# Optimization experiments

Measured on AMD Instinct MI355X. Metric: run time of the kernel, lower is better.

The kernel has to match this reference:

```python
import jax, jax.numpy as jnp
import numpy as np

B, T, H = 2, 2048, 1024
NUM_HEADS = 16
HEAD_DIM = H // NUM_HEADS
MAX_REL = 4


def setup_inputs() -> dict:
    key = jax.random.key(0)
    ks = jax.random.split(key, 12)
    s = 1.0 / np.sqrt(H)
    inp = {
        "x": jax.random.normal(ks[0], (B, T, H), dtype=jnp.float32),
        "text_mask": jax.random.randint(ks[1], (B, T), 0, 2, dtype=jnp.int32),
        "Wq": jax.random.normal(ks[2], (H, H), dtype=jnp.float32) * s,
        "bq": jnp.zeros((H,), dtype=jnp.float32),
        "Wk": jax.random.normal(ks[3], (H, H), dtype=jnp.float32) * s,
        "bk": jnp.zeros((H,), dtype=jnp.float32),
        "Wv": jax.random.normal(ks[4], (H, H), dtype=jnp.float32) * s,
        "bv": jnp.zeros((H,), dtype=jnp.float32),
        "Wo": jax.random.normal(ks[5], (H, H), dtype=jnp.float32) * s,
        "bo": jnp.zeros((H,), dtype=jnp.float32),
        "rel_bias": jax.random.normal(ks[6], (2 * MAX_REL + 1, NUM_HEADS), dtype=jnp.float32),
    }
    return inp


def reference(x, text_mask, Wq, bq, Wk, bk, Wv, bv, Wo, bo, rel_bias):
    b, t, h = x.shape
    scale = HEAD_DIM ** (-0.5)

    def proj(W, bias):
        # [b,t,h] -> [b,heads,t,head_dim]
        return (x @ W.T + bias).reshape(b, t, NUM_HEADS, HEAD_DIM).transpose(0, 2, 1, 3)

    q = proj(Wq, bq)
    k = proj(Wk, bk)
    v = proj(Wv, bv)

    scores = jnp.einsum("bhqd,bhkd->bhqk", q, k) * scale  # [b,heads,t,t]

    pos = jnp.arange(t)
    rel = jnp.clip(pos[None, :] - pos[:, None], -MAX_REL, MAX_REL) + MAX_REL  # [t,t]
    bias = rel_bias[rel]  # [t,t,heads]
    scores = scores + bias.transpose(2, 0, 1)[None]  # broadcast over batch

    key_valid = text_mask.astype(bool)  # [b,t]
    scores = jnp.where(key_valid[:, None, None, :], scores, -10000.0)

    attn = jax.nn.softmax(scores, axis=-1)
    hidden = jnp.einsum("bhqk,bhkd->bhqd", attn, v)
    hidden = hidden.transpose(0, 2, 1, 3).reshape(b, t, h)
    out = hidden @ Wo.T + bo
    return out * text_mask.astype(out.dtype)[:, :, None]
```

## Files before the change

### kernel.cpp

```cpp
#include <hip/hip_runtime.h>
#include <hip/hip_bf16.h>

#define B_ 2
#define T_ 2048
#define H_ 1024
#define NH 16
#define HD 64

typedef __attribute__((ext_vector_type(8))) short bf16x8;
typedef __attribute__((ext_vector_type(4))) short bf16x4;
typedef __attribute__((ext_vector_type(4))) float f32x4;

#define ASYNC_COPY16(gptr, lptr)                                              \
    __builtin_amdgcn_global_load_lds(                                         \
        (const __attribute__((address_space(1))) void*)(gptr),                \
        (__attribute__((address_space(3))) void*)(lptr), 16, 0, 0)

#if __has_builtin(__builtin_amdgcn_exp2f)
#define EXP2(x) __builtin_amdgcn_exp2f(x)
#else
static __device__ inline float EXP2(float x) {
    float r;
    asm volatile("v_exp_f32 %0, %1" : "=v"(r) : "v"(x));
    return r;
}
#endif

static __device__ inline unsigned short f2bf(float f) {
    union { float f; unsigned u; } v; v.f = f;
    unsigned r = v.u + 0x7fff + ((v.u >> 16) & 1);
    return (unsigned short)(r >> 16);
}

static __device__ inline unsigned pkbf(float a, float b) {
    float2 t2; t2.x = a; t2.y = b;
    __hip_bfloat162 h = __float22bfloat162_rn(t2);
    union { __hip_bfloat162 h; unsigned u; } cv; cv.h = h;
    return cv.u;
}

static __device__ inline bf16x8 mk8(unsigned a, unsigned b, unsigned c,
                                    unsigned d) {
    union { bf16x8 v; unsigned u[4]; } cv;
    cv.u[0] = a; cv.u[1] = b; cv.u[2] = c; cv.u[3] = d;
    return cv.v;
}

static __device__ inline f32x4 zero4() {
    f32x4 z = {0.f, 0.f, 0.f, 0.f};
    return z;
}

#define LOG2E 1.44269504088896f

__global__ void cvt_kernel(const float* __restrict__ x,
                           const float* __restrict__ wq,
                           const float* __restrict__ wk,
                           const float* __restrict__ wv,
                           const float* __restrict__ wo,
                           const int* __restrict__ maskp,
                           unsigned short* __restrict__ dst,
                           unsigned* __restrict__ cidx,
                           unsigned short* __restrict__ vidx,
                           unsigned short* __restrict__ maskc,
                           unsigned* __restrict__ meta,
                           float* __restrict__ outz) {
    if (blockIdx.x > 8192) {
        long long idx =
            ((long long)(blockIdx.x - 8193) * 256 + threadIdx.x) * 4;
        if (idx < 4194304LL) {
            float4 z = {0.f, 0.f, 0.f, 0.f};
            *(float4*)(outz + idx) = z;
        }
        return;
    }
    if (blockIdx.x == 8192) {
        __shared__ unsigned ps[256];
        int t = threadIdx.x;
        int base = t * 16;
        int bb = base >> 11;
        unsigned mv = 0, cnt = 0;
#pragma unroll
        for (int i = 0; i < 16; i++) {
            if (maskp[base + i]) { mv |= (1u << i); cnt++; }
        }
        ps[t] = cnt;
        __syncthreads();
        for (int off = 1; off < 128; off <<= 1) {
            unsigned add = ((t & 127) >= off) ? ps[t - off] : 0;
            __syncthreads();
            ps[t] += add;
            __syncthreads();
        }
        unsigned cnt0 = ps[127], cnt1 = ps[255];
        unsigned ex = ps[t] - cnt;
        unsigned local = ex;
        unsigned g = (bb ? cnt0 : 0) + ex;
        for (int i = 0; i < 16; i++) {
            if (mv & (1u << i)) {
                cidx[g] = (unsigned)(base + i);
                vidx[bb * 2048 + local] =
                    (unsigned short)(base + i - bb * 2048);
                maskc[bb * 2048 + local] = 0x3F80;
                g++; local++;
            }
        }
        if (t == 0) { meta[0] = cnt0; meta[1] = cnt1; meta[2] = cnt0 + cnt1; }
        __syncthreads();
        unsigned C = cnt0 + cnt1;
        for (unsigned i = C + t; i < 4224; i += 256) cidx[i] = 0;
        for (unsigned i = cnt0 + t; i < 2048; i += 256) {
            vidx[i] = 0; maskc[i] = 0;
        }
        for (unsigned i = cnt1 + t; i < 2048; i += 256) {
            vidx[2048 + i] = 0; maskc[2048 + i] = 0;
        }
        return;
    }
    long long i0 = ((long long)blockIdx.x * blockDim.x + threadIdx.x) * 4;
    const float* src; long long off;
    if (i0 < 4194304LL)      { src = x;  off = i0; }
    else if (i0 < 5242880LL) { src = wq; off = i0 - 4194304LL; }
    else if (i0 < 6291456LL) { src = wk; off = i0 - 5242880LL; }
    else if (i0 < 7340032LL) { src = wv; off = i0 - 6291456LL; }
    else                     { src = wo; off = i0 - 7340032LL; }
    float4 f = *(const float4*)(src + off);
    ushort4 o;
    o.x = f2bf(f.x); o.y = f2bf(f.y); o.z = f2bf(f.z); o.w = f2bf(f.w);
    *(ushort4*)(dst + i0) = o;
}

__global__ __launch_bounds__(256) void qkv_gemm(
    const unsigned short* __restrict__ A,
    const unsigned short* __restrict__ Bm,
    const float* __restrict__ bq, const float* __restrict__ bk,
    const float* __restrict__ bv,
    const unsigned* __restrict__ cidx, const unsigned* __restrict__ meta,
    unsigned short* __restrict__ qout, unsigned short* __restrict__ kout,
    unsigned short* __restrict__ vout) {
    const int K = 1024;
    int C  = (int)meta[2];
    int c0 = (int)meta[0];
    int m0 = blockIdx.y * 128, n0 = blockIdx.x * 128;
    if (m0 >= C) return;
    __shared__ __align__(16) unsigned short As[128 * 32];
    __shared__ __align__(16) unsigned short Bs[128 * 32];
    int t = threadIdx.x;
    int w = t >> 6, lane = t & 63;
    int wm = (w >> 1) * 64, wn = (w & 1) * 64;
    int c = lane & 15, qd = lane >> 4;

    f32x4 acc[4][4];
#pragma unroll
    for (int i = 0; i < 4; i++)
#pragma unroll
        for (int j = 0; j < 4; j++) acc[i][j] = zero4();

    int srow = t >> 2, sseg = (t & 3) * 8;
    int r1 = (int)cidx[m0 + srow];
    int r2 = (int)cidx[m0 + 64 + srow];
    const unsigned short* ag1 = A + (long long)r1 * K + sseg;
    const unsigned short* ag2 = A + (long long)r2 * K + sseg;
    const unsigned short* bg1 = Bm + (long long)(n0 + srow) * K + sseg;
    const unsigned short* bg2 = bg1 + 64LL * K;
    unsigned short* la1 = As + t * 8;
    unsigned short* la2 = As + (t + 256) * 8;
    unsigned short* lb1 = Bs + t * 8;
    unsigned short* lb2 = Bs + (t + 256) * 8;

    for (int kk = 0; kk < K; kk += 32) {
        __syncthreads();
        ASYNC_COPY16(ag1 + kk, la1);
        ASYNC_COPY16(ag2 + kk, la2);
        ASYNC_COPY16(bg1 + kk, lb1);
        ASYNC_COPY16(bg2 + kk, lb2);
        __syncthreads();
        bf16x8 af[4], bf[4];
#pragma unroll
        for (int i = 0; i < 4; i++)
            af[i] = *(const bf16x8*)(As + (wm + i * 16 + c) * 32 + qd * 8);
#pragma unroll
        for (int j = 0; j < 4; j++)
            bf[j] = *(const bf16x8*)(Bs + (wn + j * 16 + c) * 32 + qd * 8);
#pragma unroll
        for (int i = 0; i < 4; i++)
#pragma unroll
            for (int j = 0; j < 4; j++)
                acc[i][j] = __builtin_amdgcn_mfma_f32_16x16x32_bf16(
                    af[i], bf[j], acc[i][j], 0, 0, 0);
    }

    int gr[4][4];
#pragma unroll
    for (int i = 0; i < 4; i++)
#pragma unroll
        for (int r = 0; r < 4; r++) {
            int m = m0 + wm + i * 16 + qd * 4 + r;
            gr[i][r] = (m < C) ? (int)cidx[m] : -1;
        }

    const float QSCALE = 0.125f * LOG2E;
#pragma unroll
    for (int i = 0; i < 4; i++) {
        int m_base = m0 + wm + i * 16 + qd * 4;
#pragma unroll
        for (int j = 0; j < 4; j++) {
            int n = n0 + wn + j * 16 + c;
            int sel = n >> 10, within = n & 1023;
            int head = within >> 6, d = within & 63;
            if (sel == 0) {
                float ba = bq[within];
#pragma unroll
                for (int r = 0; r < 4; r++) {
                    if (gr[i][r] >= 0) {
                        int bb = gr[i][r] >> 11;
                        int loc = (m_base + r) - (bb ? c0 : 0);
                        qout[(((long long)(bb * NH + head)) * T_ + loc) * HD +
                             d] = f2bf((acc[i][j][r] + ba) * QSCALE);
                    }
                }
            } else if (sel == 1) {
                float ba = bk[within];
#pragma unroll
                for (int r = 0; r < 4; r++) {
                    if (gr[i][r] >= 0) {
                        int bb = gr[i][r] >> 11;
                        int loc = (m_base + r) - (bb ? c0 : 0);
                        kout[(((long long)(bb * NH + head)) * T_ + loc) * HD +
                             d] = f2bf(acc[i][j][r] + ba);
                    }
                }
            } else {
                float ba = bv[within];
                int g0 = gr[i][0], g3 = gr[i][3];
                int bb0 = g0 >> 11;
                int loc0 = m_base - (bb0 ? c0 : 0);
                if (g3 >= 0 && bb0 == (g3 >> 11) && ((loc0 & 3) == 0)) {
                    uint2 ov;
                    ov.x = pkbf(acc[i][j][0] + ba, acc[i][j][1] + ba);
                    ov.y = pkbf(acc[i][j][2] + ba, acc[i][j][3] + ba);
                    *(uint2*)(vout +
                              (((long long)(bb0 * NH + head)) * HD + d) * T_ +
                              loc0) = ov;
                } else {
#pragma unroll
                    for (int r = 0; r < 4; r++) {
                        if (gr[i][r] >= 0) {
                            int bb = gr[i][r] >> 11;
                            int loc = (m_base + r) - (bb ? c0 : 0);
                            vout[(((long long)(bb * NH + head)) * HD + d) *
                                     T_ +
                                 loc] = f2bf(acc[i][j][r] + ba);
                        }
                    }
                }
            }
        }
    }
}

__global__ __launch_bounds__(256) void out_gemm(
    const unsigned short* __restrict__ A,
    const unsigned short* __restrict__ Bm,
    const float* __restrict__ bo,
    const unsigned* __restrict__ cidx, const unsigned* __restrict__ meta,
    float* __restrict__ out) {
    const int K = 1024;
    int C = (int)meta[2];
    int m0 = blockIdx.y * 64, n0 = blockIdx.x * 128;
    if (m0 >= C) return;
    __shared__ __align__(16) unsigned short As[64 * 32];
    __shared__ __align__(16) unsigned short Bs[128 * 32];
    int t = threadIdx.x;
    int w = t >> 6, lane = t & 63;
    int wm = (w >> 1) * 32, wn = (w & 1) * 64;
    int c = lane & 15, qd = lane >> 4;

    f32x4 acc[2][4];
#pragma unroll
    for (int i = 0; i < 2; i++)
#pragma unroll
        for (int j = 0; j < 4; j++) acc[i][j] = zero4();

    int srow = t >> 2, sseg = (t & 3) * 8;
    int r1 = (int)cidx[m0 + srow];
    const unsigned short* ag1 = A + (long long)r1 * K + sseg;
    const unsigned short* bg1 = Bm + (long long)(n0 + srow) * K + sseg;
    const unsigned short* bg2 = bg1 + 64LL * K;
    unsigned short* la1 = As + t * 8;
    unsigned short* lb1 = Bs + t * 8;
    unsigned short* lb2 = Bs + (t + 256) * 8;

    for (int kk = 0; kk < K; kk += 32) {
        __syncthreads();
        ASYNC_COPY16(ag1 + kk, la1);
        ASYNC_COPY16(bg1 + kk, lb1);
        ASYNC_COPY16(bg2 + kk, lb2);
        __syncthreads();
        bf16x8 af[2], bf[4];
#pragma unroll
        for (int i = 0; i < 2; i++)
            af[i] = *(const bf16x8*)(As + (wm + i * 16 + c) * 32 + qd * 8);
#pragma unroll
        for (int j = 0; j < 4; j++)
            bf[j] = *(const bf16x8*)(Bs + (wn + j * 16 + c) * 32 + qd * 8);
#pragma unroll
        for (int i = 0; i < 2; i++)
#pragma unroll
            for (int j = 0; j < 4; j++)
                acc[i][j] = __builtin_amdgcn_mfma_f32_16x16x32_bf16(
                    af[i], bf[j], acc[i][j], 0, 0, 0);
    }

#pragma unroll
    for (int i = 0; i < 2; i++) {
#pragma unroll
        for (int r = 0; r < 4; r++) {
            int m = m0 + wm + i * 16 + qd * 4 + r;
            if (m < C) {
                long long g = (long long)cidx[m];
#pragma unroll
                for (int j = 0; j < 4; j++) {
                    int n = n0 + wn + j * 16 + c;
                    out[g * 1024 + n] = acc[i][j][r] + bo[n];
                }
            }
        }
    }
}

__global__ __launch_bounds__(256, 2) void attn_kernel(
    const unsigned short* __restrict__ qg,
    const unsigned short* __restrict__ kg,
    const unsigned short* __restrict__ vTg,
    const float* __restrict__ rel_bias,
    const unsigned short* __restrict__ maskc,
    const unsigned short* __restrict__ vidxg,
    const unsigned* __restrict__ meta,
    unsigned short* __restrict__ hid) {
    int hb = blockIdx.x, qt = blockIdx.y;
    int h = hb & 15, b = hb >> 4;
    int cnt = (int)meta[b];
    if (qt * 128 >= cnt) return;
    int nkt = (cnt + 63) >> 6;
    int t = threadIdx.x, w = t >> 6, lane = t & 63;
    int c = lane & 15, qd = lane >> 4;

    __shared__ __align__(16) unsigned short lk[2][64 * 72];
    __shared__ __align__(16) unsigned short lvT[2][64 * 72];
    __shared__ __align__(16) unsigned short lmk[2][64];
    __shared__ __align__(16) unsigned short lki[2][64];
    __shared__ float lrbf[16];

    if (t < 9) lrbf[t] = rel_bias[t * 16 + h] * LOG2E;
    float rb0 = rel_bias[0 * 16 + h] * LOG2E;
    float rb8 = rel_bias[8 * 16 + h] * LOG2E;

    const unsigned short* qp =
        qg + (((long long)(b * NH + h)) * T_ + qt * 128) * HD;
    const unsigned short* kp = kg + ((long long)(b * NH + h)) * T_ * HD;
    const unsigned short* vp = vTg + ((long long)(b * NH + h)) * HD * T_;

    bf16x8 qf[2][2];
#pragma unroll
    for (int mt = 0; mt < 2; mt++)
#pragma unroll
        for (int ks = 0; ks < 2; ks++)
            qf[mt][ks] = *(const bf16x8*)(qp + (w * 32 + mt * 16 + c) * HD +
                                          ks * 32 + qd * 8);

    const int imin = qt * 128 + w * 32;
    int imin_t = (int)vidxg[b * 2048 + min(imin, cnt - 1)];
    int imax_t = (int)vidxg[b * 2048 + min(imin + 31, cnt - 1)];
    int itrue[2];
#pragma unroll
    for (int mt = 0; mt < 2; mt++)
        itrue[mt] =
            (int)vidxg[b * 2048 + min(imin + mt * 16 + c, cnt - 1)];

    f32x4 o[4][2];
    f32x4 lacc[2];
#pragma unroll
    for (int dt = 0; dt < 4; dt++)
#pragma unroll
        for (int mt = 0; mt < 2; mt++) o[dt][mt] = zero4();
    lacc[0] = zero4(); lacc[1] = zero4();

    int srow = t >> 2, sseg = (t & 3) * 16;
    int rr = srow & 15, hf = (srow >> 4) & 1;
    int gk = (srow & 32) + (rr >> 2) * 8 + hf * 4 + (rr & 3);
    const unsigned short* kst = kp + gk * HD + sseg;
    const unsigned short* vst = vp + srow * T_ + sseg;
    const unsigned short* mst = maskc + b * 2048 + t;
    const unsigned short* ist = vidxg + b * 2048 + t * 8;

    uint4 rk0 = *(const uint4*)(kst);
    uint4 rk1 = *(const uint4*)(kst + 8);
    uint4 rv0 = *(const uint4*)(vst);
    uint4 rv1 = *(const uint4*)(vst + 8);
    unsigned short rm = (t < 64) ? *mst : 0;
    uint4 rki = {0, 0, 0, 0};
    if (t < 8) rki = *(const uint4*)(ist);

    for (int kt = 0; kt < nkt; kt++) {
        unsigned short* KB = lk[kt & 1];
        unsigned short* VB = lvT[kt & 1];
        unsigned short* MK = lmk[kt & 1];
        unsigned short* KI = lki[kt & 1];
        *(uint4*)(KB + srow * 72 + sseg)     = rk0;
        *(uint4*)(KB + srow * 72 + sseg + 8) = rk1;
        *(uint4*)(VB + srow * 72 + sseg)     = rv0;
        *(uint4*)(VB + srow * 72 + sseg + 8) = rv1;
        if (t < 64) MK[t] = rm;
        if (t < 8) *(uint4*)(KI + t * 8) = rki;
        {
            int ktn = (kt < nkt - 1) ? kt + 1 : nkt - 1;
            rk0 = *(const uint4*)(kst + ktn * 64 * HD);
            rk1 = *(const uint4*)(kst + ktn * 64 * HD + 8);
            rv0 = *(const uint4*)(vst + ktn * 64);
            rv1 = *(const uint4*)(vst + ktn * 64 + 8);
            if (t < 64) rm = mst[ktn * 64];
            if (t < 8) rki = *(const uint4*)(ist + ktn * 64);
        }
        __syncthreads();

        int j0 = kt * 64;
        int jlo_t = (int)KI[0];
        int jhi_t = (int)KI[min(63, cnt - 1 - j0)];
        bool far_lo = (jhi_t <= imin_t - 4);
        bool far_hi = (jlo_t >= imax_t + 4);
        float ub = far_lo ? rb0 : rb8;
        bool nearband = !(far_lo || far_hi);

#pragma unroll
        for (int jp = 0; jp < 2; jp++) {
            int jb = jp * 32;
            const unsigned short* kbase = KB + (jb + c) * 72 + qd * 8;
            bf16x8 kfA0 = *(const bf16x8*)(kbase);
            bf16x8 kfA1 = *(const bf16x8*)(kbase + 32);
            bf16x8 kfB0 = *(const bf16x8*)(kbase + 16 * 72);
            bf16x8 kfB1 = *(const bf16x8*)(kbase + 16 * 72 + 32);
            bf16x8 m8 = *(const bf16x8*)(MK + jb + qd * 8);
            ushort4 kivA = *(const ushort4*)(KI + jb + qd * 8);
            ushort4 kivB = *(const ushort4*)(KI + jb + qd * 8 + 4);
            bf16x8 vf[4];
#pragma unroll
            for (int dt = 0; dt < 4; dt++)
                vf[dt] = *(const bf16x8*)(VB + (dt * 16 + c) * 72 + jb +
                                          qd * 8);
#pragma unroll
            for (int mt = 0; mt < 2; mt++) {
                f32x4 accA = zero4(), accB = zero4();
                accA = __builtin_amdgcn_mfma_f32_16x16x32_bf16(
                    kfA0, qf[mt][0], accA, 0, 0, 0);
                accA = __builtin_amdgcn_mfma_f32_16x16x32_bf16(
                    kfA1, qf[mt][1], accA, 0, 0, 0);
                accB = __builtin_amdgcn_mfma_f32_16x16x32_bf16(
                    kfB0, qf[mt][0], accB, 0, 0, 0);
                accB = __builtin_amdgcn_mfma_f32_16x16x32_bf16(
                    kfB1, qf[mt][1], accB, 0, 0, 0);
                float pA0, pA1, pA2, pA3, pB0, pB1, pB2, pB3;
                if (nearband) {
                    int it = itrue[mt];
                    int a0 = (int)kivA.x - it;
                    a0 = a0 < -4 ? -4 : (a0 > 4 ? 4 : a0);
                    int a1 = (int)kivA.y - it;
                    a1 = a1 < -4 ? -4 : (a1 > 4 ? 4 : a1);
                    int a2 = (int)kivA.z - it;
                    a2 = a2 < -4 ? -4 : (a2 > 4 ? 4 : a2);
                    int a3 = (int)kivA.w - it;
                    a3 = a3 < -4 ? -4 : (a3 > 4 ? 4 : a3);
                    int b0i = (int)kivB.x - it;
                    b0i = b0i < -4 ? -4 : (b0i > 4 ? 4 : b0i);
                    int b1i = (int)kivB.y - it;
                    b1i = b1i < -4 ? -4 : (b1i > 4 ? 4 : b1i);
                    int b2i = (int)kivB.z - it;
                    b2i = b2i < -4 ? -4 : (b2i > 4 ? 4 : b2i);
                    int b3i = (int)kivB.w - it;
                    b3i = b3i < -4 ? -4 : (b3i > 4 ? 4 : b3i);
                    pA0 = EXP2(accA[0] + lrbf[a0 + 4]);
                    pA1 = EXP2(accA[1] + lrbf[a1 + 4]);
                    pA2 = EXP2(accA[2] + lrbf[a2 + 4]);
                    pA3 = EXP2(accA[3] + lrbf[a3 + 4]);
                    pB0 = EXP2(accB[0] + lrbf[b0i + 4]);
                    pB1 = EXP2(accB[1] + lrbf[b1i + 4]);
                    pB2 = EXP2(accB[2] + lrbf[b2i + 4]);
                    pB3 = EXP2(accB[3] + lrbf[b3i + 4]);
                } else {
                    pA0 = EXP2(accA[0] + ub);
                    pA1 = EXP2(accA[1] + ub);
                    pA2 = EXP2(accA[2] + ub);
                    pA3 = EXP2(accA[3] + ub);
                    pB0 = EXP2(accB[0] + ub);
                    pB1 = EXP2(accB[1] + ub);
                    pB2 = EXP2(accB[2] + ub);
                    pB3 = EXP2(accB[3] + ub);
                }
                bf16x8 pf = mk8(pkbf(pA0, pA1), pkbf(pA2, pA3),
                                pkbf(pB0, pB1), pkbf(pB2, pB3));
                lacc[mt] = __builtin_amdgcn_mfma_f32_16x16x32_bf16(
                    m8, pf, lacc[mt], 0, 0, 0);
#pragma unroll
                for (int dt = 0; dt < 4; dt++)
                    o[dt][mt] = __builtin_amdgcn_mfma_f32_16x16x32_bf16(
                        vf[dt], pf, o[dt][mt], 0, 0, 0);
            }
        }
    }

#pragma unroll
    for (int mt = 0; mt < 2; mt++) {
        int rc = imin + mt * 16 + c;
        if (rc < cnt) {
            float invl = 1.0f / lacc[mt][0];
            long long row = (long long)b * T_ + itrue[mt];
#pragma unroll
            for (int dt = 0; dt < 4; dt++) {
                uint2 ov;
                ov.x = pkbf(o[dt][mt][0] * invl, o[dt][mt][1] * invl);
                ov.y = pkbf(o[dt][mt][2] * invl, o[dt][mt][3] * invl);
                *(uint2*)(hid + row * H_ + h * HD + dt * 16 + qd * 4) = ov;
            }
        }
    }
}

extern "C" void kernel_launch(void* const* d_in, const int* in_sizes, int n_in,
                              void* d_out, int out_size, void* d_ws,
                              size_t ws_size, hipStream_t stream) {
    const float* x    = (const float*)d_in[0];
    const int* maskp  = (const int*)d_in[1];
    const float* Wq   = (const float*)d_in[2];
    const float* bq   = (const float*)d_in[3];
    const float* Wk   = (const float*)d_in[4];
    const float* bk   = (const float*)d_in[5];
    const float* Wv   = (const float*)d_in[6];
    const float* bv   = (const float*)d_in[7];
    const float* Wo   = (const float*)d_in[8];
    const float* bo   = (const float*)d_in[9];
    const float* rb   = (const float*)d_in[10];
    float* out        = (float*)d_out;

    unsigned short* ws = (unsigned short*)d_ws;
    unsigned short* xb    = ws;
    unsigned short* wqkv  = ws + 4194304LL;
    unsigned short* wo_b  = ws + 7340032LL;
    unsigned short* qb    = ws + 8388608LL;
    unsigned short* kb    = ws + 12582912LL;
    unsigned short* vTb   = ws + 16777216LL;
    unsigned short* hid   = ws + 20971520LL;
    unsigned* meta        = (unsigned*)(ws + 25165824LL);
    unsigned* cidx        = (unsigned*)(ws + 25165856LL);
    unsigned short* vidx  = ws + 25174304LL;
    unsigned short* maskc = ws + 25178400LL;

    cvt_kernel<<<12289, 256, 0, stream>>>(x, Wq, Wk, Wv, Wo, maskp, ws, cidx,
                                          vidx, maskc, meta, out);
    qkv_gemm<<<dim3(24, 32), 256, 0, stream>>>(xb, wqkv, bq, bk, bv, cidx,
                                               meta, qb, kb, vTb);
    attn_kernel<<<dim3(32, 16), 256, 0, stream>>>(qb, kb, vTb, rb, maskc,
                                                  vidx, meta, hid);
    out_gemm<<<dim3(8, 64), 256, 0, stream>>>(hid, wo_b, bo, cidx, meta,
                                              out);
}
```

Measured before the change: 188.9 us.

## Double-buffer GEMM LDS tiles with K=64 stages and shrink QKV M-tile

Measured after the change: 191.0 us. About the same (+1.1%).

```diff
diff --git a/kernel.cpp b/kernel.cpp
--- a/kernel.cpp
+++ b/kernel.cpp
@@ -141,58 +141,68 @@
     const int K = 1024;
     int C  = (int)meta[2];
     int c0 = (int)meta[0];
-    int m0 = blockIdx.y * 128, n0 = blockIdx.x * 128;
+    int m0 = blockIdx.y * 64, n0 = blockIdx.x * 128;
     if (m0 >= C) return;
-    __shared__ __align__(16) unsigned short As[128 * 32];
-    __shared__ __align__(16) unsigned short Bs[128 * 32];
+    __shared__ __align__(16) unsigned short As[2][2][64 * 32];
+    __shared__ __align__(16) unsigned short Bs[2][2][128 * 32];
     int t = threadIdx.x;
     int w = t >> 6, lane = t & 63;
-    int wm = (w >> 1) * 64, wn = (w & 1) * 64;
+    int wm = (w >> 1) * 32, wn = (w & 1) * 64;
     int c = lane & 15, qd = lane >> 4;
 
-    f32x4 acc[4][4];
-#pragma unroll
-    for (int i = 0; i < 4; i++)
+    f32x4 acc[2][4];
+#pragma unroll
+    for (int i = 0; i < 2; i++)
 #pragma unroll
         for (int j = 0; j < 4; j++) acc[i][j] = zero4();
 
     int srow = t >> 2, sseg = (t & 3) * 8;
     int r1 = (int)cidx[m0 + srow];
-    int r2 = (int)cidx[m0 + 64 + srow];
     const unsigned short* ag1 = A + (long long)r1 * K + sseg;
-    const unsigned short* ag2 = A + (long long)r2 * K + sseg;
     const unsigned short* bg1 = Bm + (long long)(n0 + srow) * K + sseg;
     const unsigned short* bg2 = bg1 + 64LL * K;
-    unsigned short* la1 = As + t * 8;
-    unsigned short* la2 = As + (t + 256) * 8;
-    unsigned short* lb1 = Bs + t * 8;
-    unsigned short* lb2 = Bs + (t + 256) * 8;
-
-    for (int kk = 0; kk < K; kk += 32) {
+
+#define QKV_STAGE(buf, kk)                                                    \
+    do {                                                                      \
+        ASYNC_COPY16(ag1 + (kk),      &As[buf][0][t * 8]);                    \
+        ASYNC_COPY16(ag1 + (kk) + 32, &As[buf][1][t * 8]);                    \
+        ASYNC_COPY16(bg1 + (kk),      &Bs[buf][0][t * 8]);                    \
+        ASYNC_COPY16(bg1 + (kk) + 32, &Bs[buf][1][t * 8]);                    \
+        ASYNC_COPY16(bg2 + (kk),      &Bs[buf][0][2048 + t * 8]);             \
+        ASYNC_COPY16(bg2 + (kk) + 32, &Bs[buf][1][2048 + t * 8]);             \
+    } while (0)
+
+    QKV_STAGE(0, 0);
+    __syncthreads();
+    int cur = 0;
+    for (int step = 0; step < 16; step++) {
+        if (step < 15) QKV_STAGE(cur ^ 1, (step + 1) * 64);
+#pragma unroll
+        for (int p = 0; p < 2; p++) {
+            bf16x8 af[2], bf[4];
+#pragma unroll
+            for (int i = 0; i < 2; i++)
+                af[i] = *(const bf16x8*)(&As[cur][p][(wm + i * 16 + c) * 32 +
+                                                     qd * 8]);
+#pragma unroll
+            for (int j = 0; j < 4; j++)
+                bf[j] = *(const bf16x8*)(&Bs[cur][p][(wn + j * 16 + c) * 32 +
+                                                     qd * 8]);
+#pragma unroll
+            for (int i = 0; i < 2; i++)
+#pragma unroll
+                for (int j = 0; j < 4; j++)
+                    acc[i][j] = __builtin_amdgcn_mfma_f32_16x16x32_bf16(
+                        af[i], bf[j], acc[i][j], 0, 0, 0);
+        }
         __syncthreads();
-        ASYNC_COPY16(ag1 + kk, la1);
-        ASYNC_COPY16(ag2 + kk, la2);
-        ASYNC_COPY16(bg1 + kk, lb1);
-        ASYNC_COPY16(bg2 + kk, lb2);
-        __syncthreads();
-        bf16x8 af[4], bf[4];
-#pragma unroll
-        for (int i = 0; i < 4; i++)
-            af[i] = *(const bf16x8*)(As + (wm + i * 16 + c) * 32 + qd * 8);
-#pragma unroll
-        for (int j = 0; j < 4; j++)
-            bf[j] = *(const bf16x8*)(Bs + (wn + j * 16 + c) * 32 + qd * 8);
-#pragma unroll
-        for (int i = 0; i < 4; i++)
-#pragma unroll
-            for (int j = 0; j < 4; j++)
-                acc[i][j] = __builtin_amdgcn_mfma_f32_16x16x32_bf16(
-                    af[i], bf[j], acc[i][j], 0, 0, 0);
-    }
-
-    int gr[4][4];
-#pragma unroll
-    for (int i = 0; i < 4; i++)
+        cur ^= 1;
+    }
+#undef QKV_STAGE
+
+    int gr[2][4];
+#pragma unroll
+    for (int i = 0; i < 2; i++)
 #pragma unroll
         for (int r = 0; r < 4; r++) {
             int m = m0 + wm + i * 16 + qd * 4 + r;
@@ -201,7 +211,7 @@
 
     const float QSCALE = 0.125f * LOG2E;
 #pragma unroll
-    for (int i = 0; i < 4; i++) {
+    for (int i = 0; i < 2; i++) {
         int m_base = m0 + wm + i * 16 + qd * 4;
 #pragma unroll
         for (int j = 0; j < 4; j++) {
@@ -269,8 +279,8 @@
     int C = (int)meta[2];
     int m0 = blockIdx.y * 64, n0 = blockIdx.x * 128;
     if (m0 >= C) return;
-    __shared__ __align__(16) unsigned short As[64 * 32];
-    __shared__ __align__(16) unsigned short Bs[128 * 32];
+    __shared__ __align__(16) unsigned short As[2][2][64 * 32];
+    __shared__ __align__(16) unsigned short Bs[2][2][128 * 32];
     int t = threadIdx.x;
     int w = t >> 6, lane = t & 63;
     int wm = (w >> 1) * 32, wn = (w & 1) * 64;
@@ -287,30 +297,44 @@
     const unsigned short* ag1 = A + (long long)r1 * K + sseg;
     const unsigned short* bg1 = Bm + (long long)(n0 + srow) * K + sseg;
     const unsigned short* bg2 = bg1 + 64LL * K;
-    unsigned short* la1 = As + t * 8;
-    unsigned short* lb1 = Bs + t * 8;
-    unsigned short* lb2 = Bs + (t + 256) * 8;
-
-    for (int kk = 0; kk < K; kk += 32) {
+
+#define OUT_STAGE(buf, kk)                                                    \
+    do {                                                                      \
+        ASYNC_COPY16(ag1 + (kk),      &As[buf][0][t * 8]);                    \
+        ASYNC_COPY16(ag1 + (kk) + 32, &As[buf][1][t * 8]);                    \
+        ASYNC_COPY16(bg1 + (kk),      &Bs[buf][0][t * 8]);                    \
+        ASYNC_COPY16(bg1 + (kk) + 32, &Bs[buf][1][t * 8]);                    \
+        ASYNC_COPY16(bg2 + (kk),      &Bs[buf][0][2048 + t * 8]);             \
+        ASYNC_COPY16(bg2 + (kk) + 32, &Bs[buf][1][2048 + t * 8]);             \
+    } while (0)
+
+    OUT_STAGE(0, 0);
+    __syncthreads();
+    int cur = 0;
+    for (int step = 0; step < 16; step++) {
+        if (step < 15) OUT_STAGE(cur ^ 1, (step + 1) * 64);
+#pragma unroll
+        for (int p = 0; p < 2; p++) {
+            bf16x8 af[2], bf[4];
+#pragma unroll
+            for (int i = 0; i < 2; i++)
+                af[i] = *(const bf16x8*)(&As[cur][p][(wm + i * 16 + c) * 32 +
+                                                     qd * 8]);
+#pragma unroll
+            for (int j = 0; j < 4; j++)
+                bf[j] = *(const bf16x8*)(&Bs[cur][p][(wn + j * 16 + c) * 32 +
+                                                     qd * 8]);
+#pragma unroll
+            for (int i = 0; i < 2; i++)
+#pragma unroll
+                for (int j = 0; j < 4; j++)
+                    acc[i][j] = __builtin_amdgcn_mfma_f32_16x16x32_bf16(
+                        af[i], bf[j], acc[i][j], 0, 0, 0);
+        }
         __syncthreads();
-        ASYNC_COPY16(ag1 + kk, la1);
-        ASYNC_COPY16(bg1 + kk, lb1);
-        ASYNC_COPY16(bg2 + kk, lb2);
-        __syncthreads();
-        bf16x8 af[2], bf[4];
-#pragma unroll
-        for (int i = 0; i < 2; i++)
-            af[i] = *(const bf16x8*)(As + (wm + i * 16 + c) * 32 + qd * 8);
-#pragma unroll
-        for (int j = 0; j < 4; j++)
-            bf[j] = *(const bf16x8*)(Bs + (wn + j * 16 + c) * 32 + qd * 8);
-#pragma unroll
-        for (int i = 0; i < 2; i++)
-#pragma unroll
-            for (int j = 0; j < 4; j++)
-                acc[i][j] = __builtin_amdgcn_mfma_f32_16x16x32_bf16(
-                    af[i], bf[j], acc[i][j], 0, 0, 0);
-    }
+        cur ^= 1;
+    }
+#undef OUT_STAGE
 
 #pragma unroll
     for (int i = 0; i < 2; i++) {
@@ -556,7 +580,7 @@
 
     cvt_kernel<<<12289, 256, 0, stream>>>(x, Wq, Wk, Wv, Wo, maskp, ws, cidx,
                                           vidx, maskc, meta, out);
-    qkv_gemm<<<dim3(24, 32), 256, 0, stream>>>(xb, wqkv, bq, bk, bv, cidx,
+    qkv_gemm<<<dim3(24, 64), 256, 0, stream>>>(xb, wqkv, bq, bk, bv, cidx,
                                                meta, qb, kb, vTb);
     attn_kernel<<<dim3(32, 16), 256, 0, stream>>>(qb, kb, vTb, rb, maskc,
                                                   vidx, meta, hid);
```
